# Kernel tuning notes

Hardware: AMD Instinct MI355X
Metric: run time of the kernel (lower is better)

The kernel has to match this reference:

```python
import jax, jax.numpy as jnp
import numpy as np

B, S, D = 8, 4096, 256


def setup_inputs() -> dict:
    key = jax.random.key(0)
    kq, kk, kv, kb = jax.random.split(key, 4)
    q = jax.random.normal(kq, (B, S, D), dtype=jnp.float32)
    k = jax.random.normal(kk, (B, S, D), dtype=jnp.float32)
    v = jax.random.normal(kv, (B, S, D), dtype=jnp.float32)
    beta = jax.random.uniform(kb, (B, S), dtype=jnp.float32)
    return {"q": q, "k": k, "v": v, "beta": beta}


def reference(q, k, v, beta):
    # Delta-rule linear attention recurrence:
    #   h_t = beta_t * h_{t-1} + k_t^T v_t   (h: [B, D, D])
    #   o_t = q_t @ h_t                      (o: [B, D])
    dtype = q.dtype
    b, s, d = q.shape
    h0 = jnp.zeros((b, d, d), dtype=dtype)

    def step(h, inp):
        q_t, k_t, v_t, b_t = inp  # q_t/k_t/v_t: [B, D], b_t: [B]
        h = h * b_t[:, None, None] + jnp.einsum('bi,bj->bij', k_t, v_t)
        o_t = jnp.einsum('bi,bij->bj', q_t, h)
        return h, o_t

    xs = (q.transpose(1, 0, 2), k.transpose(1, 0, 2),
          v.transpose(1, 0, 2), beta.T)  # time-major
    _, out = jax.lax.scan(step, h0, xs)  # out: [S, B, D]
    return out.transpose(1, 0, 2)  # [B, S, D]
```

## Files before the change

### kernel.cpp

```cpp
#include <hip/hip_runtime.h>
#include <hip/hip_bf16.h>
#include <math.h>


#define B_ 8
#define S_ 4096
#define D_ 256
#define L_ 128
#define C_ (S_ / L_)
#define BC_ (B_ * C_)
#define STK 66

typedef __attribute__((ext_vector_type(8))) short s8v;
typedef __attribute__((ext_vector_type(4))) float f4v;
typedef unsigned short u16;
typedef unsigned int u32;

__device__ __forceinline__ u32 pk2(float lo, float hi) {
  union { __hip_bfloat162 h; u32 u; } cv;
  cv.h = __float22bfloat162_rn(make_float2(lo, hi));
  return cv.u;
}
__device__ __forceinline__ s8v pack8(const float4 a, const float4 b) {
  union { u32 u[4]; s8v v; } r;
  r.u[0] = pk2(a.x, a.y); r.u[1] = pk2(a.z, a.w);
  r.u[2] = pk2(b.x, b.y); r.u[3] = pk2(b.z, b.w);
  return r.v;
}

__device__ __forceinline__ void beta_scan128(const float* betap, float* ls,
                                             int tid) {
  if (tid < 64) {
    float x = log2f(fmaxf(betap[tid], 1e-30f));
#pragma unroll
    for (int off = 1; off < 64; off <<= 1) {
      float y = __shfl_up(x, off);
      if (tid >= off) x += y;
    }
    ls[tid] = x;
    const float tot0 = __shfl(x, 63);
    float z = log2f(fmaxf(betap[64 + tid], 1e-30f));
#pragma unroll
    for (int off = 1; off < 64; off <<= 1) {
      float y = __shfl_up(z, off);
      if (tid >= off) z += y;
    }
    ls[64 + tid] = z + tot0;
  }
}

__global__ __launch_bounds__(512, 2) void ks_summary6(
    const float* __restrict__ kg, const float* __restrict__ vg,
    const float* __restrict__ beta, u16* __restrict__ A,
    float* __restrict__ P)
{
  __shared__ float ls[L_];
  __shared__ __align__(16) u16 U[2][256 * STK];
  __shared__ __align__(16) u16 BN[64 * 264];

  const int bc = blockIdx.x;
  const int b = bc / C_, c = bc % C_;
  const int tid = threadIdx.x;
  const float* betap = beta + (size_t)b * S_ + (size_t)c * L_;
  const float* kbase = kg + ((size_t)b * S_ + (size_t)c * L_) * D_;
  const float* vbase = vg + ((size_t)b * S_ + (size_t)c * L_) * D_;

  beta_scan128(betap, ls, tid);
  __syncthreads();
  const float ltot = ls[L_ - 1];
  if (tid == 0) P[bc] = exp2f(ltot);

  const int hh = tid >> 8;
  const int t2 = tid & 255;
  const int iLs = t2 & 7;
  const int s0s = (t2 >> 3) * 2;
  const int sg = hh * 64 + s0s;

  {
    const float* src0 = kbase + (size_t)sg * D_;
    const float* src1 = src0 + D_;
    const float w0 = exp2f(ltot - ls[sg]);
    const float w1 = exp2f(ltot - ls[sg + 1]);
    u16* dst = U[hh];
#pragma unroll
    for (int p = 0; p < 8; ++p) {
      const int i0 = p * 32 + iLs * 4;
      float a0[4], a1[4];
      *(float4*)a0 = *(const float4*)(src0 + i0);
      *(float4*)a1 = *(const float4*)(src1 + i0);
#pragma unroll
      for (int u = 0; u < 4; ++u)
        *(u32*)&dst[(i0 + u) * STK + s0s] = pk2(a0[u] * w0, a1[u] * w1);
    }
  }
  __syncthreads();

  const int lane = tid & 63, wave = tid >> 6;
  const int quad = lane >> 4, l15 = lane & 15;
  const int i0w = wave * 32;

  s8v af[2][4];
#pragma unroll
  for (int mt = 0; mt < 2; ++mt)
#pragma unroll
    for (int ks = 0; ks < 4; ++ks)
      af[mt][ks] = *(const s8v*)&U[ks >> 1][(i0w + mt * 16 + l15) * STK +
                                            (ks & 1) * 32 + quad * 8];
  __syncthreads();

  {
    const float* src0 = vbase + (size_t)sg * D_;
    const float* src1 = src0 + D_;
    u16* dst = U[hh];
#pragma unroll
    for (int p = 0; p < 8; ++p) {
      const int i0 = p * 32 + iLs * 4;
      float a0[4], a1[4];
      *(float4*)a0 = *(const float4*)(src0 + i0);
      *(float4*)a1 = *(const float4*)(src1 + i0);
#pragma unroll
      for (int u = 0; u < 4; ++u)
        *(u32*)&dst[(i0 + u) * STK + s0s] = pk2(a0[u], a1[u]);
    }
  }
  __syncthreads();

  u16* Ab = A + (size_t)bc * D_ * D_;

  for (int ng = 0; ng < 4; ++ng) {
    f4v acc[2][4];
#pragma unroll
    for (int mt = 0; mt < 2; ++mt)
#pragma unroll
      for (int nt = 0; nt < 4; ++nt) acc[mt][nt] = (f4v){0.f, 0.f, 0.f, 0.f};

#pragma unroll
    for (int ks = 0; ks < 4; ++ks) {
      const int so = (ks & 1) * 32 + quad * 8;
      s8v bv[4];
#pragma unroll
      for (int nt = 0; nt < 4; ++nt)
        bv[nt] = *(const s8v*)&U[ks >> 1][(ng * 64 + nt * 16 + l15) * STK + so];
#pragma unroll
      for (int mt = 0; mt < 2; ++mt)
#pragma unroll
        for (int nt = 0; nt < 4; ++nt)
          acc[mt][nt] = __builtin_amdgcn_mfma_f32_16x16x32_bf16(
              af[mt][ks], bv[nt], acc[mt][nt], 0, 0, 0);
    }
#pragma unroll
    for (int mt = 0; mt < 2; ++mt)
#pragma unroll
      for (int nt = 0; nt < 4; ++nt) {
        const int jl = nt * 16 + l15;
        uint2 w;
        w.x = pk2(acc[mt][nt][0], acc[mt][nt][1]);
        w.y = pk2(acc[mt][nt][2], acc[mt][nt][3]);
        *(uint2*)&BN[jl * 264 + i0w + mt * 16 + quad * 4] = w;
      }
    __syncthreads();
    {
      const int jl = tid >> 3;
      const int il = (tid & 7) * 8;
#pragma unroll
      for (int p = 0; p < 4; ++p) {
        const int iu = il + p * 64;
        *(s8v*)&Ab[(size_t)(ng * 64 + jl) * D_ + iu] =
            *(const s8v*)&BN[jl * 264 + iu];
      }
    }
    __syncthreads();
  }
}

__global__ __launch_bounds__(256) void ks_scan6(
    u16* __restrict__ A, const float* __restrict__ P)
{
  const int g = blockIdx.x;
  const int b = g >> 6;
  const int unit = ((g & 63) << 8) + threadIdx.x;
  u16* base = A + (size_t)b * ((size_t)C_ * D_ * D_) + (size_t)unit * 4;
  const float* Pb = P + b * C_;

  uint2 d[C_];
#pragma unroll
  for (int c = 0; c < C_; ++c)
    d[c] = *(const uint2*)(base + (size_t)c * (D_ * D_));

  float h0 = 0.f, h1 = 0.f, h2 = 0.f, h3 = 0.f;
#pragma unroll
  for (int c = 0; c < C_; ++c) {
    const float pc = Pb[c];
    const uint2 u = d[c];
    const float a0 = __uint_as_float(u.x << 16);
    const float a1 = __uint_as_float(u.x & 0xFFFF0000u);
    const float a2 = __uint_as_float(u.y << 16);
    const float a3 = __uint_as_float(u.y & 0xFFFF0000u);
    d[c].x = pk2(h0, h1);
    d[c].y = pk2(h2, h3);
    h0 = fmaf(pc, h0, a0); h1 = fmaf(pc, h1, a1);
    h2 = fmaf(pc, h2, a2); h3 = fmaf(pc, h3, a3);
  }
#pragma unroll
  for (int c = 0; c < C_; ++c)
    *(uint2*)(base + (size_t)c * (D_ * D_)) = d[c];
}

__global__ __launch_bounds__(512, 2) void ks_output6(
    const float* __restrict__ qg, const float* __restrict__ kg,
    const float* __restrict__ vg, const float* __restrict__ beta,
    const u16* __restrict__ Hg, float* __restrict__ outg)
{
  __shared__ float ls[L_];
  __shared__ float cv[L_];
  __shared__ __align__(16) u16 QB[L_ * 264];
  __shared__ __align__(16) u16 Tm[L_ * 136];
  __shared__ __align__(16) u16 VT[256 * STK];

  const int bc = blockIdx.x;
  const int b = bc / C_, c = bc % C_;
  const int tid = threadIdx.x;
  const float* betap = beta + (size_t)b * S_ + (size_t)c * L_;
  const float* qbase = qg + ((size_t)b * S_ + (size_t)c * L_) * D_;
  const float* kbase = kg + ((size_t)b * S_ + (size_t)c * L_) * D_;
  const float* vbase = vg + ((size_t)b * S_ + (size_t)c * L_) * D_;
  const u16* Hb = Hg + (size_t)bc * D_ * D_;

  beta_scan128(betap, ls, tid);

  {
    const int t = tid >> 2;
    const int cg = (tid & 3) * 8;
    const float* src = qbase + (size_t)t * D_ + cg;
#pragma unroll
    for (int p = 0; p < 8; ++p) {
      const s8v pk = pack8(*(const float4*)(src + p * 32),
                           *(const float4*)(src + p * 32 + 4));
      *(s8v*)&QB[t * 264 + cg + p * 32] = pk;
    }
  }
  __syncthreads();
  if (tid < L_) cv[tid] = exp2f(ls[tid]);

  const int lane = tid & 63, wave = tid >> 6;
  const int quad = lane >> 4, l15 = lane & 15;
  const int j0w = wave * 32;

  {
    const int mA = wave * 16;
    f4v accA[8];
#pragma unroll
    for (int i = 0; i < 8; ++i) accA[i] = (f4v){0.f, 0.f, 0.f, 0.f};
#pragma unroll
    for (int kd = 0; kd < 8; ++kd) {
      const int d0 = kd * 32 + quad * 8;
      const float* krow = kbase + (size_t)(mA + l15) * D_ + d0;
      const s8v af = pack8(*(const float4*)krow, *(const float4*)(krow + 4));
#pragma unroll
      for (int nt = 0; nt < 8; ++nt) {
        const s8v bf = *(const s8v*)&QB[(nt * 16 + l15) * 264 + d0];
        accA[nt] = __builtin_amdgcn_mfma_f32_16x16x32_bf16(af, bf, accA[nt],
                                                           0, 0, 0);
      }
    }
#pragma unroll
    for (int nt = 0; nt < 8; ++nt) {
      const int t = nt * 16 + l15;
      const float lt = ls[t];
      const int s0 = mA + quad * 4;
      float v[4];
#pragma unroll
      for (int r = 0; r < 4; ++r) {
        const int s = s0 + r;
        v[r] = (s <= t) ? accA[nt][r] * exp2f(lt - ls[s]) : 0.f;
      }
      uint2 w;
      w.x = pk2(v[0], v[1]);
      w.y = pk2(v[2], v[3]);
      *(uint2*)&Tm[t * 136 + s0] = w;
    }
  }

  {
    const int iL = tid & 15;
    const int s0 = ((tid >> 4) & 31) * 2;
    const float* src0 = vbase + (size_t)s0 * D_;
    const float* src1 = src0 + D_;
#pragma unroll
    for (int p = 0; p < 4; ++p) {
      const int i0 = p * 64 + iL * 4;
      float a0[4], a1[4];
      *(float4*)a0 = *(const float4*)(src0 + i0);
      *(float4*)a1 = *(const float4*)(src1 + i0);
#pragma unroll
      for (int u = 0; u < 4; ++u)
        *(u32*)&VT[(i0 + u) * STK + s0] = pk2(a0[u], a1[u]);
    }
  }

  s8v hc[2];
#pragma unroll
  for (int mt = 0; mt < 2; ++mt)
    hc[mt] = *(const s8v*)(Hb + (size_t)(j0w + mt * 16 + l15) * D_ + quad * 8);

  __syncthreads();

  f4v acc[2][8];
#pragma unroll
  for (int mt = 0; mt < 2; ++mt)
#pragma unroll
    for (int nt = 0; nt < 8; ++nt) acc[mt][nt] = (f4v){0.f, 0.f, 0.f, 0.f};

#pragma unroll
  for (int ks = 0; ks < 8; ++ks) {
    const int io = ks * 32 + quad * 8;
    s8v hn[2] = {hc[0], hc[1]};
    if (ks < 7) {
#pragma unroll
      for (int mt = 0; mt < 2; ++mt)
        hn[mt] = *(const s8v*)(Hb + (size_t)(j0w + mt * 16 + l15) * D_ +
                               io + 32);
    }
    s8v bf[8];
#pragma unroll
    for (int nt = 0; nt < 8; ++nt)
      bf[nt] = *(const s8v*)&QB[(nt * 16 + l15) * 264 + io];
#pragma unroll
    for (int mt = 0; mt < 2; ++mt)
#pragma unroll
      for (int nt = 0; nt < 8; ++nt)
        acc[mt][nt] = __builtin_amdgcn_mfma_f32_16x16x32_bf16(
            hc[mt], bf[nt], acc[mt][nt], 0, 0, 0);
    hc[0] = hn[0]; hc[1] = hn[1];
  }
#pragma unroll
  for (int nt = 0; nt < 8; ++nt) {
    const float ct = cv[nt * 16 + l15];
#pragma unroll
    for (int mt = 0; mt < 2; ++mt) {
      acc[mt][nt][0] *= ct; acc[mt][nt][1] *= ct;
      acc[mt][nt][2] *= ct; acc[mt][nt][3] *= ct;
    }
  }

#pragma unroll
  for (int ks = 0; ks < 2; ++ks) {
    const int so = ks * 32 + quad * 8;
    s8v af[2], bf[8];
#pragma unroll
    for (int mt = 0; mt < 2; ++mt)
      af[mt] = *(const s8v*)&VT[(j0w + mt * 16 + l15) * STK + so];
#pragma unroll
    for (int nt = 0; nt < 8; ++nt)
      bf[nt] = *(const s8v*)&Tm[(nt * 16 + l15) * 136 + so];
#pragma unroll
    for (int mt = 0; mt < 2; ++mt)
#pragma unroll
      for (int nt = 0; nt < 8; ++nt)
        acc[mt][nt] = __builtin_amdgcn_mfma_f32_16x16x32_bf16(
            af[mt], bf[nt], acc[mt][nt], 0, 0, 0);
  }

  __syncthreads();
  {
    const int iL = tid & 15;
    const int s0 = ((tid >> 4) & 31) * 2;
    const float* src0 = vbase + (size_t)(64 + s0) * D_;
    const float* src1 = src0 + D_;
#pragma unroll
    for (int p = 0; p < 4; ++p) {
      const int i0 = p * 64 + iL * 4;
      float a0[4], a1[4];
      *(float4*)a0 = *(const float4*)(src0 + i0);
      *(float4*)a1 = *(const float4*)(src1 + i0);
#pragma unroll
      for (int u = 0; u < 4; ++u)
        *(u32*)&VT[(i0 + u) * STK + s0] = pk2(a0[u], a1[u]);
    }
  }
  __syncthreads();
#pragma unroll
  for (int ks = 0; ks < 2; ++ks) {
    const int so = ks * 32 + quad * 8;
    s8v af[2], bf[8];
#pragma unroll
    for (int mt = 0; mt < 2; ++mt)
      af[mt] = *(const s8v*)&VT[(j0w + mt * 16 + l15) * STK + so];
#pragma unroll
    for (int nt = 0; nt < 8; ++nt)
      bf[nt] = *(const s8v*)&Tm[(nt * 16 + l15) * 136 + 64 + so];
#pragma unroll
    for (int mt = 0; mt < 2; ++mt)
#pragma unroll
      for (int nt = 0; nt < 8; ++nt)
        acc[mt][nt] = __builtin_amdgcn_mfma_f32_16x16x32_bf16(
            af[mt], bf[nt], acc[mt][nt], 0, 0, 0);
  }

  float* ob = outg + ((size_t)b * S_ + (size_t)c * L_) * D_;
#pragma unroll
  for (int mt = 0; mt < 2; ++mt)
#pragma unroll
    for (int nt = 0; nt < 8; ++nt) {
      const int t = nt * 16 + l15;
      const int j0 = j0w + mt * 16 + quad * 4;
      float4 o;
      o.x = acc[mt][nt][0]; o.y = acc[mt][nt][1];
      o.z = acc[mt][nt][2]; o.w = acc[mt][nt][3];
      *(float4*)(ob + (size_t)t * D_ + j0) = o;
    }
}

extern "C" void kernel_launch(void* const* d_in, const int* in_sizes, int n_in,
                              void* d_out, int out_size, void* d_ws,
                              size_t ws_size, hipStream_t stream) {
  const float* q = (const float*)d_in[0];
  const float* k = (const float*)d_in[1];
  const float* v = (const float*)d_in[2];
  const float* beta = (const float*)d_in[3];
  float* out = (float*)d_out;

  u16* A = (u16*)d_ws;
  float* P = (float*)((char*)d_ws + (size_t)BC_ * D_ * D_ * sizeof(u16));

  ks_summary6<<<dim3(BC_), dim3(512), 0, stream>>>(k, v, beta, A, P);
  ks_scan6<<<dim3(512), dim3(256), 0, stream>>>(A, P);
  ks_output6<<<dim3(BC_), dim3(512), 0, stream>>>(q, k, v, beta, A, out);
}
```

Baseline: 172.3 us.

## Fuse summary, scan and output stages into one cooperative kernel with grid syncs

The three kernels (per-chunk state summary, cross-chunk scan, output) are merged into a single cooperatively launched kernel that uses grid.sync between phases. Global loads of k, v and q are issued early into registers so they overlap with the beta scan and the grid barriers. This removes two kernel launches and lets each block keep its beta prefix and inputs across phases. In exchange it adds heavy register pressure from the prefetch arrays, needs all 256 blocks co-resident, and pays for two grid-wide barriers.

Result: slower. 260.2 us (+51.0%).

```diff
diff --git a/kernel.cpp b/kernel.cpp
--- a/kernel.cpp
+++ b/kernel.cpp
@@ -1,6 +1,9 @@
 #include <hip/hip_runtime.h>
 #include <hip/hip_bf16.h>
+#include <hip/hip_cooperative_groups.h>
 #include <math.h>
+
+namespace cg = cooperative_groups;
 
 
 #define B_ 8
@@ -28,194 +31,18 @@
   return r.v;
 }
 
-__device__ __forceinline__ void beta_scan128(const float* betap, float* ls,
-                                             int tid) {
-  if (tid < 64) {
-    float x = log2f(fmaxf(betap[tid], 1e-30f));
-#pragma unroll
-    for (int off = 1; off < 64; off <<= 1) {
-      float y = __shfl_up(x, off);
-      if (tid >= off) x += y;
-    }
-    ls[tid] = x;
-    const float tot0 = __shfl(x, 63);
-    float z = log2f(fmaxf(betap[64 + tid], 1e-30f));
-#pragma unroll
-    for (int off = 1; off < 64; off <<= 1) {
-      float y = __shfl_up(z, off);
-      if (tid >= off) z += y;
-    }
-    ls[64 + tid] = z + tot0;
-  }
-}
-
-__global__ __launch_bounds__(512, 2) void ks_summary6(
-    const float* __restrict__ kg, const float* __restrict__ vg,
-    const float* __restrict__ beta, u16* __restrict__ A,
-    float* __restrict__ P)
-{
-  __shared__ float ls[L_];
-  __shared__ __align__(16) u16 U[2][256 * STK];
-  __shared__ __align__(16) u16 BN[64 * 264];
-
-  const int bc = blockIdx.x;
-  const int b = bc / C_, c = bc % C_;
-  const int tid = threadIdx.x;
-  const float* betap = beta + (size_t)b * S_ + (size_t)c * L_;
-  const float* kbase = kg + ((size_t)b * S_ + (size_t)c * L_) * D_;
-  const float* vbase = vg + ((size_t)b * S_ + (size_t)c * L_) * D_;
-
-  beta_scan128(betap, ls, tid);
-  __syncthreads();
-  const float ltot = ls[L_ - 1];
-  if (tid == 0) P[bc] = exp2f(ltot);
-
-  const int hh = tid >> 8;
-  const int t2 = tid & 255;
-  const int iLs = t2 & 7;
-  const int s0s = (t2 >> 3) * 2;
-  const int sg = hh * 64 + s0s;
-
-  {
-    const float* src0 = kbase + (size_t)sg * D_;
-    const float* src1 = src0 + D_;
-    const float w0 = exp2f(ltot - ls[sg]);
-    const float w1 = exp2f(ltot - ls[sg + 1]);
-    u16* dst = U[hh];
-#pragma unroll
-    for (int p = 0; p < 8; ++p) {
-      const int i0 = p * 32 + iLs * 4;
-      float a0[4], a1[4];
-      *(float4*)a0 = *(const float4*)(src0 + i0);
-      *(float4*)a1 = *(const float4*)(src1 + i0);
-#pragma unroll
-      for (int u = 0; u < 4; ++u)
-        *(u32*)&dst[(i0 + u) * STK + s0s] = pk2(a0[u] * w0, a1[u] * w1);
-    }
-  }
-  __syncthreads();
-
-  const int lane = tid & 63, wave = tid >> 6;
-  const int quad = lane >> 4, l15 = lane & 15;
-  const int i0w = wave * 32;
-
-  s8v af[2][4];
-#pragma unroll
-  for (int mt = 0; mt < 2; ++mt)
-#pragma unroll
-    for (int ks = 0; ks < 4; ++ks)
-      af[mt][ks] = *(const s8v*)&U[ks >> 1][(i0w + mt * 16 + l15) * STK +
-                                            (ks & 1) * 32 + quad * 8];
-  __syncthreads();
-
-  {
-    const float* src0 = vbase + (size_t)sg * D_;
-    const float* src1 = src0 + D_;
-    u16* dst = U[hh];
-#pragma unroll
-    for (int p = 0; p < 8; ++p) {
-      const int i0 = p * 32 + iLs * 4;
-      float a0[4], a1[4];
-      *(float4*)a0 = *(const float4*)(src0 + i0);
-      *(float4*)a1 = *(const float4*)(src1 + i0);
-#pragma unroll
-      for (int u = 0; u < 4; ++u)
-        *(u32*)&dst[(i0 + u) * STK + s0s] = pk2(a0[u], a1[u]);
-    }
-  }
-  __syncthreads();
-
-  u16* Ab = A + (size_t)bc * D_ * D_;
-
-  for (int ng = 0; ng < 4; ++ng) {
-    f4v acc[2][4];
-#pragma unroll
-    for (int mt = 0; mt < 2; ++mt)
-#pragma unroll
-      for (int nt = 0; nt < 4; ++nt) acc[mt][nt] = (f4v){0.f, 0.f, 0.f, 0.f};
-
-#pragma unroll
-    for (int ks = 0; ks < 4; ++ks) {
-      const int so = (ks & 1) * 32 + quad * 8;
-      s8v bv[4];
-#pragma unroll
-      for (int nt = 0; nt < 4; ++nt)
-        bv[nt] = *(const s8v*)&U[ks >> 1][(ng * 64 + nt * 16 + l15) * STK + so];
-#pragma unroll
-      for (int mt = 0; mt < 2; ++mt)
-#pragma unroll
-        for (int nt = 0; nt < 4; ++nt)
-          acc[mt][nt] = __builtin_amdgcn_mfma_f32_16x16x32_bf16(
-              af[mt][ks], bv[nt], acc[mt][nt], 0, 0, 0);
-    }
-#pragma unroll
-    for (int mt = 0; mt < 2; ++mt)
-#pragma unroll
-      for (int nt = 0; nt < 4; ++nt) {
-        const int jl = nt * 16 + l15;
-        uint2 w;
-        w.x = pk2(acc[mt][nt][0], acc[mt][nt][1]);
-        w.y = pk2(acc[mt][nt][2], acc[mt][nt][3]);
-        *(uint2*)&BN[jl * 264 + i0w + mt * 16 + quad * 4] = w;
-      }
-    __syncthreads();
-    {
-      const int jl = tid >> 3;
-      const int il = (tid & 7) * 8;
-#pragma unroll
-      for (int p = 0; p < 4; ++p) {
-        const int iu = il + p * 64;
-        *(s8v*)&Ab[(size_t)(ng * 64 + jl) * D_ + iu] =
-            *(const s8v*)&BN[jl * 264 + iu];
-      }
-    }
-    __syncthreads();
-  }
-}
-
-__global__ __launch_bounds__(256) void ks_scan6(
-    u16* __restrict__ A, const float* __restrict__ P)
-{
-  const int g = blockIdx.x;
-  const int b = g >> 6;
-  const int unit = ((g & 63) << 8) + threadIdx.x;
-  u16* base = A + (size_t)b * ((size_t)C_ * D_ * D_) + (size_t)unit * 4;
-  const float* Pb = P + b * C_;
-
-  uint2 d[C_];
-#pragma unroll
-  for (int c = 0; c < C_; ++c)
-    d[c] = *(const uint2*)(base + (size_t)c * (D_ * D_));
-
-  float h0 = 0.f, h1 = 0.f, h2 = 0.f, h3 = 0.f;
-#pragma unroll
-  for (int c = 0; c < C_; ++c) {
-    const float pc = Pb[c];
-    const uint2 u = d[c];
-    const float a0 = __uint_as_float(u.x << 16);
-    const float a1 = __uint_as_float(u.x & 0xFFFF0000u);
-    const float a2 = __uint_as_float(u.y << 16);
-    const float a3 = __uint_as_float(u.y & 0xFFFF0000u);
-    d[c].x = pk2(h0, h1);
-    d[c].y = pk2(h2, h3);
-    h0 = fmaf(pc, h0, a0); h1 = fmaf(pc, h1, a1);
-    h2 = fmaf(pc, h2, a2); h3 = fmaf(pc, h3, a3);
-  }
-#pragma unroll
-  for (int c = 0; c < C_; ++c)
-    *(uint2*)(base + (size_t)c * (D_ * D_)) = d[c];
-}
-
-__global__ __launch_bounds__(512, 2) void ks_output6(
+#define SM_WORDS 68096
+
+__global__ __launch_bounds__(512, 2) void ks_fused(
     const float* __restrict__ qg, const float* __restrict__ kg,
     const float* __restrict__ vg, const float* __restrict__ beta,
-    const u16* __restrict__ Hg, float* __restrict__ outg)
+    u16* __restrict__ A, float* __restrict__ P, float* __restrict__ outg)
 {
+  __shared__ __align__(16) u16 smraw[SM_WORDS];
   __shared__ float ls[L_];
   __shared__ float cv[L_];
-  __shared__ __align__(16) u16 QB[L_ * 264];
-  __shared__ __align__(16) u16 Tm[L_ * 136];
-  __shared__ __align__(16) u16 VT[256 * STK];
+
+  cg::grid_group grid = cg::this_grid();
 
   const int bc = blockIdx.x;
   const int b = bc / C_, c = bc % C_;
@@ -224,26 +51,213 @@
   const float* qbase = qg + ((size_t)b * S_ + (size_t)c * L_) * D_;
   const float* kbase = kg + ((size_t)b * S_ + (size_t)c * L_) * D_;
   const float* vbase = vg + ((size_t)b * S_ + (size_t)c * L_) * D_;
-  const u16* Hb = Hg + (size_t)bc * D_ * D_;
-
-  beta_scan128(betap, ls, tid);
-
-  {
-    const int t = tid >> 2;
-    const int cg = (tid & 3) * 8;
-    const float* src = qbase + (size_t)t * D_ + cg;
-#pragma unroll
-    for (int p = 0; p < 8; ++p) {
-      const s8v pk = pack8(*(const float4*)(src + p * 32),
-                           *(const float4*)(src + p * 32 + 4));
-      *(s8v*)&QB[t * 264 + cg + p * 32] = pk;
-    }
-  }
-  __syncthreads();
-  if (tid < L_) cv[tid] = exp2f(ls[tid]);
 
   const int lane = tid & 63, wave = tid >> 6;
   const int quad = lane >> 4, l15 = lane & 15;
+
+  const int hh = tid >> 8;
+  const int t2 = tid & 255;
+  const int iLs = t2 & 7;
+  const int s0s = (t2 >> 3) * 2;
+  const int sg = hh * 64 + s0s;
+
+  float bx0 = 1.f, bx1 = 1.f;
+  if (tid < 64) { bx0 = betap[tid]; bx1 = betap[64 + tid]; }
+
+  float4 kp[16], vp[16];
+  {
+    const float* k0 = kbase + (size_t)sg * D_;
+    const float* v0 = vbase + (size_t)sg * D_;
+#pragma unroll
+    for (int p = 0; p < 8; ++p) {
+      const int i0 = p * 32 + iLs * 4;
+      kp[2 * p]     = *(const float4*)(k0 + i0);
+      kp[2 * p + 1] = *(const float4*)(k0 + D_ + i0);
+    }
+#pragma unroll
+    for (int p = 0; p < 8; ++p) {
+      const int i0 = p * 32 + iLs * 4;
+      vp[2 * p]     = *(const float4*)(v0 + i0);
+      vp[2 * p + 1] = *(const float4*)(v0 + D_ + i0);
+    }
+  }
+
+  if (tid < 64) {
+    float x = log2f(fmaxf(bx0, 1e-30f));
+#pragma unroll
+    for (int off = 1; off < 64; off <<= 1) {
+      float y = __shfl_up(x, off);
+      if (tid >= off) x += y;
+    }
+    ls[tid] = x;
+    const float tot0 = __shfl(x, 63);
+    float z = log2f(fmaxf(bx1, 1e-30f));
+#pragma unroll
+    for (int off = 1; off < 64; off <<= 1) {
+      float y = __shfl_up(z, off);
+      if (tid >= off) z += y;
+    }
+    ls[64 + tid] = z + tot0;
+  }
+  __syncthreads();
+  const float ltot = ls[L_ - 1];
+  if (tid == 0) P[bc] = exp2f(ltot);
+  if (tid < L_) cv[tid] = exp2f(ls[tid]);
+
+  {
+    const float w0 = exp2f(ltot - ls[sg]);
+    const float w1 = exp2f(ltot - ls[sg + 1]);
+    u16* dst = smraw + hh * 16896;
+#pragma unroll
+    for (int p = 0; p < 8; ++p) {
+      const int i0 = p * 32 + iLs * 4;
+      const float4 a0 = kp[2 * p], a1 = kp[2 * p + 1];
+      *(u32*)&dst[(i0 + 0) * STK + s0s] = pk2(a0.x * w0, a1.x * w1);
+      *(u32*)&dst[(i0 + 1) * STK + s0s] = pk2(a0.y * w0, a1.y * w1);
+      *(u32*)&dst[(i0 + 2) * STK + s0s] = pk2(a0.z * w0, a1.z * w1);
+      *(u32*)&dst[(i0 + 3) * STK + s0s] = pk2(a0.w * w0, a1.w * w1);
+    }
+  }
+  __syncthreads();
+
+  const int i0w = wave * 32;
+  s8v af[2][4];
+#pragma unroll
+  for (int mt = 0; mt < 2; ++mt)
+#pragma unroll
+    for (int ks = 0; ks < 4; ++ks)
+      af[mt][ks] = *(const s8v*)&smraw[(ks >> 1) * 16896 +
+          (i0w + mt * 16 + l15) * STK + (ks & 1) * 32 + quad * 8];
+  __syncthreads();
+
+  {
+    u16* dst = smraw + hh * 16896;
+#pragma unroll
+    for (int p = 0; p < 8; ++p) {
+      const int i0 = p * 32 + iLs * 4;
+      const float4 a0 = vp[2 * p], a1 = vp[2 * p + 1];
+      *(u32*)&dst[(i0 + 0) * STK + s0s] = pk2(a0.x, a1.x);
+      *(u32*)&dst[(i0 + 1) * STK + s0s] = pk2(a0.y, a1.y);
+      *(u32*)&dst[(i0 + 2) * STK + s0s] = pk2(a0.z, a1.z);
+      *(u32*)&dst[(i0 + 3) * STK + s0s] = pk2(a0.w, a1.w);
+    }
+  }
+  __syncthreads();
+
+  u16* Ab = A + (size_t)bc * D_ * D_;
+  for (int ng = 0; ng < 4; ++ng) {
+    f4v acc[2][4];
+#pragma unroll
+    for (int mt = 0; mt < 2; ++mt)
+#pragma unroll
+      for (int nt = 0; nt < 4; ++nt) acc[mt][nt] = (f4v){0.f, 0.f, 0.f, 0.f};
+
+#pragma unroll
+    for (int ks = 0; ks < 4; ++ks) {
+      const int so = (ks & 1) * 32 + quad * 8;
+      s8v bv[4];
+#pragma unroll
+      for (int nt = 0; nt < 4; ++nt)
+        bv[nt] = *(const s8v*)&smraw[(ks >> 1) * 16896 +
+                                     (ng * 64 + nt * 16 + l15) * STK + so];
+#pragma unroll
+      for (int mt = 0; mt < 2; ++mt)
+#pragma unroll
+        for (int nt = 0; nt < 4; ++nt)
+          acc[mt][nt] = __builtin_amdgcn_mfma_f32_16x16x32_bf16(
+              af[mt][ks], bv[nt], acc[mt][nt], 0, 0, 0);
+    }
+    u16* BNb = smraw + 33792 + (ng & 1) * 16896;
+#pragma unroll
+    for (int mt = 0; mt < 2; ++mt)
+#pragma unroll
+      for (int nt = 0; nt < 4; ++nt) {
+        const int jl = nt * 16 + l15;
+        uint2 w;
+        w.x = pk2(acc[mt][nt][0], acc[mt][nt][1]);
+        w.y = pk2(acc[mt][nt][2], acc[mt][nt][3]);
+        *(uint2*)&BNb[jl * 264 + i0w + mt * 16 + quad * 4] = w;
+      }
+    __syncthreads();
+    {
+      const int jl = tid >> 3;
+      const int il = (tid & 7) * 8;
+#pragma unroll
+      for (int p = 0; p < 4; ++p) {
+        const int iu = il + p * 64;
+        *(s8v*)&Ab[(size_t)(ng * 64 + jl) * D_ + iu] =
+            *(const s8v*)&BNb[jl * 264 + iu];
+      }
+    }
+  }
+
+  const int qt = tid >> 2, qc = (tid & 3) * 8;
+  float4 qp[16];
+  {
+    const float* src = qbase + (size_t)qt * D_ + qc;
+#pragma unroll
+    for (int p = 0; p < 8; ++p) {
+      qp[2 * p]     = *(const float4*)(src + p * 32);
+      qp[2 * p + 1] = *(const float4*)(src + p * 32 + 4);
+    }
+  }
+
+  grid.sync();
+
+  {
+    const int b2 = bc >> 5;
+    u16* base2 = A + (size_t)b2 * ((size_t)C_ * D_ * D_) +
+                 (size_t)(((bc & 31) << 9) + tid) * 4;
+    const float* Pb = P + b2 * C_;
+
+    uint2 d[C_];
+#pragma unroll
+    for (int cc = 0; cc < C_; ++cc)
+      d[cc] = *(const uint2*)(base2 + (size_t)cc * (D_ * D_));
+
+    u16* QB = smraw;
+#pragma unroll
+    for (int p = 0; p < 8; ++p)
+      *(s8v*)&QB[qt * 264 + qc + p * 32] = pack8(qp[2 * p], qp[2 * p + 1]);
+
+    float h0 = 0.f, h1 = 0.f, h2 = 0.f, h3 = 0.f;
+#pragma unroll
+    for (int cc = 0; cc < C_; ++cc) {
+      const float pc = Pb[cc];
+      const uint2 u = d[cc];
+      const float a0 = __uint_as_float(u.x << 16);
+      const float a1 = __uint_as_float(u.x & 0xFFFF0000u);
+      const float a2 = __uint_as_float(u.y << 16);
+      const float a3 = __uint_as_float(u.y & 0xFFFF0000u);
+      d[cc].x = pk2(h0, h1);
+      d[cc].y = pk2(h2, h3);
+      h0 = fmaf(pc, h0, a0); h1 = fmaf(pc, h1, a1);
+      h2 = fmaf(pc, h2, a2); h3 = fmaf(pc, h3, a3);
+    }
+#pragma unroll
+    for (int cc = 0; cc < C_; ++cc)
+      *(uint2*)(base2 + (size_t)cc * (D_ * D_)) = d[cc];
+  }
+
+  const int iL3 = tid & 15;
+  const int s03 = ((tid >> 4) & 31) * 2;
+  float4 vp0[8];
+  {
+    const float* a0 = vbase + (size_t)s03 * D_;
+#pragma unroll
+    for (int p = 0; p < 4; ++p) {
+      const int i0 = p * 64 + iL3 * 4;
+      vp0[2 * p]     = *(const float4*)(a0 + i0);
+      vp0[2 * p + 1] = *(const float4*)(a0 + D_ + i0);
+    }
+  }
+
+  grid.sync();
+
+  u16* QB = smraw;
+  u16* Tm = smraw + 33792;
+  u16* VT = smraw + 51200;
+  const u16* Hb = A + (size_t)bc * D_ * D_;
   const int j0w = wave * 32;
 
   {
@@ -255,11 +269,11 @@
     for (int kd = 0; kd < 8; ++kd) {
       const int d0 = kd * 32 + quad * 8;
       const float* krow = kbase + (size_t)(mA + l15) * D_ + d0;
-      const s8v af = pack8(*(const float4*)krow, *(const float4*)(krow + 4));
+      const s8v afr = pack8(*(const float4*)krow, *(const float4*)(krow + 4));
 #pragma unroll
       for (int nt = 0; nt < 8; ++nt) {
         const s8v bf = *(const s8v*)&QB[(nt * 16 + l15) * 264 + d0];
-        accA[nt] = __builtin_amdgcn_mfma_f32_16x16x32_bf16(af, bf, accA[nt],
+        accA[nt] = __builtin_amdgcn_mfma_f32_16x16x32_bf16(afr, bf, accA[nt],
                                                            0, 0, 0);
       }
     }
@@ -268,33 +282,28 @@
       const int t = nt * 16 + l15;
       const float lt = ls[t];
       const int s0 = mA + quad * 4;
-      float v[4];
+      float v4[4];
 #pragma unroll
       for (int r = 0; r < 4; ++r) {
         const int s = s0 + r;
-        v[r] = (s <= t) ? accA[nt][r] * exp2f(lt - ls[s]) : 0.f;
+        v4[r] = (s <= t) ? accA[nt][r] * exp2f(lt - ls[s]) : 0.f;
       }
       uint2 w;
-      w.x = pk2(v[0], v[1]);
-      w.y = pk2(v[2], v[3]);
+      w.x = pk2(v4[0], v4[1]);
+      w.y = pk2(v4[2], v4[3]);
       *(uint2*)&Tm[t * 136 + s0] = w;
     }
   }
 
   {
-    const int iL = tid & 15;
-    const int s0 = ((tid >> 4) & 31) * 2;
-    const float* src0 = vbase + (size_t)s0 * D_;
-    const float* src1 = src0 + D_;
 #pragma unroll
     for (int p = 0; p < 4; ++p) {
-      const int i0 = p * 64 + iL * 4;
-      float a0[4], a1[4];
-      *(float4*)a0 = *(const float4*)(src0 + i0);
-      *(float4*)a1 = *(const float4*)(src1 + i0);
-#pragma unroll
-      for (int u = 0; u < 4; ++u)
-        *(u32*)&VT[(i0 + u) * STK + s0] = pk2(a0[u], a1[u]);
+      const int i0 = p * 64 + iL3 * 4;
+      const float4 a0 = vp0[2 * p], a1 = vp0[2 * p + 1];
+      *(u32*)&VT[(i0 + 0) * STK + s03] = pk2(a0.x, a1.x);
+      *(u32*)&VT[(i0 + 1) * STK + s03] = pk2(a0.y, a1.y);
+      *(u32*)&VT[(i0 + 2) * STK + s03] = pk2(a0.z, a1.z);
+      *(u32*)&VT[(i0 + 3) * STK + s03] = pk2(a0.w, a1.w);
     }
   }
 
@@ -304,6 +313,17 @@
     hc[mt] = *(const s8v*)(Hb + (size_t)(j0w + mt * 16 + l15) * D_ + quad * 8);
 
   __syncthreads();
+
+  float4 vp1[8];
+  {
+    const float* b0 = vbase + (size_t)(64 + s03) * D_;
+#pragma unroll
+    for (int p = 0; p < 4; ++p) {
+      const int i0 = p * 64 + iL3 * 4;
+      vp1[2 * p]     = *(const float4*)(b0 + i0);
+      vp1[2 * p + 1] = *(const float4*)(b0 + D_ + i0);
+    }
+  }
 
   f4v acc[2][8];
 #pragma unroll
@@ -321,16 +341,16 @@
         hn[mt] = *(const s8v*)(Hb + (size_t)(j0w + mt * 16 + l15) * D_ +
                                io + 32);
     }
-    s8v bf[8];
+    s8v bfq[8];
 #pragma unroll
     for (int nt = 0; nt < 8; ++nt)
-      bf[nt] = *(const s8v*)&QB[(nt * 16 + l15) * 264 + io];
+      bfq[nt] = *(const s8v*)&QB[(nt * 16 + l15) * 264 + io];
 #pragma unroll
     for (int mt = 0; mt < 2; ++mt)
 #pragma unroll
       for (int nt = 0; nt < 8; ++nt)
         acc[mt][nt] = __builtin_amdgcn_mfma_f32_16x16x32_bf16(
-            hc[mt], bf[nt], acc[mt][nt], 0, 0, 0);
+            hc[mt], bfq[nt], acc[mt][nt], 0, 0, 0);
     hc[0] = hn[0]; hc[1] = hn[1];
   }
 #pragma unroll
@@ -346,55 +366,50 @@
 #pragma unroll
   for (int ks = 0; ks < 2; ++ks) {
     const int so = ks * 32 + quad * 8;
-    s8v af[2], bf[8];
-#pragma unroll
-    for (int mt = 0; mt < 2; ++mt)
-      af[mt] = *(const s8v*)&VT[(j0w + mt * 16 + l15) * STK + so];
+    s8v afv[2], bfv[8];
+#pragma unroll
+    for (int mt = 0; mt < 2; ++mt)
+      afv[mt] = *(const s8v*)&VT[(j0w + mt * 16 + l15) * STK + so];
 #pragma unroll
     for (int nt = 0; nt < 8; ++nt)
-      bf[nt] = *(const s8v*)&Tm[(nt * 16 + l15) * 136 + so];
+      bfv[nt] = *(const s8v*)&Tm[(nt * 16 + l15) * 136 + so];
 #pragma unroll
     for (int mt = 0; mt < 2; ++mt)
 #pragma unroll
       for (int nt = 0; nt < 8; ++nt)
         acc[mt][nt] = __builtin_amdgcn_mfma_f32_16x16x32_bf16(
-            af[mt], bf[nt], acc[mt][nt], 0, 0, 0);
-  }
-
-  __syncthreads();
-  {
-    const int iL = tid & 15;
-    const int s0 = ((tid >> 4) & 31) * 2;
-    const float* src0 = vbase + (size_t)(64 + s0) * D_;
-    const float* src1 = src0 + D_;
+            afv[mt], bfv[nt], acc[mt][nt], 0, 0, 0);
+  }
+
+  __syncthreads();
+  {
 #pragma unroll
     for (int p = 0; p < 4; ++p) {
-      const int i0 = p * 64 + iL * 4;
-      float a0[4], a1[4];
-      *(float4*)a0 = *(const float4*)(src0 + i0);
-      *(float4*)a1 = *(const float4*)(src1 + i0);
-#pragma unroll
-      for (int u = 0; u < 4; ++u)
-        *(u32*)&VT[(i0 + u) * STK + s0] = pk2(a0[u], a1[u]);
+      const int i0 = p * 64 + iL3 * 4;
+      const float4 a0 = vp1[2 * p], a1 = vp1[2 * p + 1];
+      *(u32*)&VT[(i0 + 0) * STK + s03] = pk2(a0.x, a1.x);
+      *(u32*)&VT[(i0 + 1) * STK + s03] = pk2(a0.y, a1.y);
+      *(u32*)&VT[(i0 + 2) * STK + s03] = pk2(a0.z, a1.z);
+      *(u32*)&VT[(i0 + 3) * STK + s03] = pk2(a0.w, a1.w);
     }
   }
   __syncthreads();
 #pragma unroll
   for (int ks = 0; ks < 2; ++ks) {
     const int so = ks * 32 + quad * 8;
-    s8v af[2], bf[8];
-#pragma unroll
-    for (int mt = 0; mt < 2; ++mt)
-      af[mt] = *(const s8v*)&VT[(j0w + mt * 16 + l15) * STK + so];
+    s8v afv[2], bfv[8];
+#pragma unroll
+    for (int mt = 0; mt < 2; ++mt)
+      afv[mt] = *(const s8v*)&VT[(j0w + mt * 16 + l15) * STK + so];
 #pragma unroll
     for (int nt = 0; nt < 8; ++nt)
-      bf[nt] = *(const s8v*)&Tm[(nt * 16 + l15) * 136 + 64 + so];
+      bfv[nt] = *(const s8v*)&Tm[(nt * 16 + l15) * 136 + 64 + so];
 #pragma unroll
     for (int mt = 0; mt < 2; ++mt)
 #pragma unroll
       for (int nt = 0; nt < 8; ++nt)
         acc[mt][nt] = __builtin_amdgcn_mfma_f32_16x16x32_bf16(
-            af[mt], bf[nt], acc[mt][nt], 0, 0, 0);
+            afv[mt], bfv[nt], acc[mt][nt], 0, 0, 0);
   }
 
   float* ob = outg + ((size_t)b * S_ + (size_t)c * L_) * D_;
@@ -423,7 +438,8 @@
   u16* A = (u16*)d_ws;
   float* P = (float*)((char*)d_ws + (size_t)BC_ * D_ * D_ * sizeof(u16));
 
-  ks_summary6<<<dim3(BC_), dim3(512), 0, stream>>>(k, v, beta, A, P);
-  ks_scan6<<<dim3(512), dim3(256), 0, stream>>>(A, P);
-  ks_output6<<<dim3(BC_), dim3(512), 0, stream>>>(q, k, v, beta, A, out);
+  void* args[] = {(void*)&q, (void*)&k, (void*)&v, (void*)&beta,
+                  (void*)&A, (void*)&P, (void*)&out};
+  hipLaunchCooperativeKernel((const void*)ks_fused, dim3(BC_), dim3(512),
+                             args, 0, stream);
 }
```
